# Performance work log

Measured on AMD Instinct MI355X. Metric: run time of the kernel, lower is better.

Reference implementation:

```python
import jax, jax.numpy as jnp
import numpy as np

BN_EPS = 1e-5

def _conv1x1(h, w, b):
    # h: [N, Cin, L], w: [Cout, Cin], b: [Cout] -> [N, Cout, L]
    return jnp.einsum('ncl,oc->nol', h, w) + b[None, :, None]

def _bn_eval(h, g, bt, m, v):
    return (h - m[None, :, None]) / jnp.sqrt(v[None, :, None] + BN_EPS) * g[None, :, None] + bt[None, :, None]

def setup_inputs() -> dict:
    key = jax.random.key(0)
    ks = jax.random.split(key, 20)
    B, R, L, F = 1024, 16, 12, 16
    num_cat, num_cont, V, D = 8, 8, 1000, 32
    FD = F * D  # 512
    H1, H2 = 64, 32
    s = 0.05
    idx_part = jax.random.randint(ks[0], (B, R, L, num_cat), 0, V).astype(jnp.float32)
    cont_part = jax.random.normal(ks[1], (B, R, L, num_cont), dtype=jnp.float32)
    x = jnp.concatenate([idx_part, cont_part], axis=-1)
    return {
        'x': x,
        'cat_emb': jax.random.normal(ks[2], (num_cat, V, D), dtype=jnp.float32) * s,
        'cat_lin': jax.random.normal(ks[3], (num_cat, V, D), dtype=jnp.float32) * s,
        'cont_w': jax.random.normal(ks[4], (num_cont, D), dtype=jnp.float32) * s,
        'cont_b': jax.random.normal(ks[5], (num_cont, D), dtype=jnp.float32) * s,
        'cont_lin_w': jax.random.normal(ks[6], (num_cont, D), dtype=jnp.float32) * s,
        'cont_lin_b': jax.random.normal(ks[7], (num_cont, D), dtype=jnp.float32) * s,
        'fin_bias': jnp.zeros((D,), dtype=jnp.float32),
        'dnn1_w': jax.random.normal(ks[8], (H1, FD), dtype=jnp.float32) * s,
        'dnn1_b': jnp.zeros((H1,), dtype=jnp.float32),
        'bn1_g': jnp.ones((H1,), dtype=jnp.float32),
        'bn1_bt': jnp.zeros((H1,), dtype=jnp.float32),
        'bn1_m': jnp.zeros((H1,), dtype=jnp.float32),
        'bn1_v': jnp.ones((H1,), dtype=jnp.float32),
        'dnn2_w': jax.random.normal(ks[9], (H2, H1), dtype=jnp.float32) * s,
        'dnn2_b': jnp.zeros((H2,), dtype=jnp.float32),
        'bn2_g': jnp.ones((H2,), dtype=jnp.float32),
        'bn2_bt': jnp.zeros((H2,), dtype=jnp.float32),
        'bn2_m': jnp.zeros((H2,), dtype=jnp.float32),
        'bn2_v': jnp.ones((H2,), dtype=jnp.float32),
        'out_w': jax.random.normal(ks[10], (D, H2), dtype=jnp.float32) * s,
        'out_b': jnp.zeros((D,), dtype=jnp.float32),
    }

def reference(x, cat_emb, cat_lin, cont_w, cont_b, cont_lin_w, cont_lin_b, fin_bias,
              dnn1_w, dnn1_b, bn1_g, bn1_bt, bn1_m, bn1_v,
              dnn2_w, dnn2_b, bn2_g, bn2_bt, bn2_m, bn2_v,
              out_w, out_b):
    B, R, L, F = x.shape
    N = B * R
    num_cat = cat_emb.shape[0]
    D = cat_emb.shape[2]
    xf = x.reshape(N, L, F)
    idx = xf[:, :, :num_cat].astype(jnp.int32)   # [N, L, C]
    cont = xf[:, :, num_cat:]                    # [N, L, J]
    f_ids = jnp.arange(num_cat)[None, None, :]   # broadcast field ids
    # embedding path -> [N, D, field, L]
    cat_e = cat_emb[f_ids, idx].transpose(0, 3, 2, 1)                                   # [N,D,C,L]
    cont_e = (cont[..., None] * cont_w[None, None] + cont_b[None, None]).transpose(0, 3, 2, 1)  # [N,D,J,L]
    emb_all = jnp.concatenate([cat_e, cont_e], axis=2)                                  # [N,D,F,L]
    # FM second-order interaction
    ssum = emb_all.sum(axis=2)
    fm = 0.5 * (ssum * ssum - (emb_all * emb_all).sum(axis=2))                          # [N,D,L]
    # linear terms
    cat_l = cat_lin[f_ids, idx].transpose(0, 3, 2, 1)
    cont_l = (cont[..., None] * cont_lin_w[None, None] + cont_lin_b[None, None]).transpose(0, 3, 2, 1)
    linear_terms = cat_l.sum(axis=2) + cont_l.sum(axis=2) + fin_bias[None, :, None]     # [N,D,L]
    # DNN over field-major concatenated channels [N, F*D, L]
    dnn_in = emb_all.transpose(0, 2, 1, 3).reshape(N, F * D, L)
    h = jax.nn.relu(_bn_eval(_conv1x1(dnn_in, dnn1_w, dnn1_b), bn1_g, bn1_bt, bn1_m, bn1_v))
    h = jax.nn.relu(_bn_eval(_conv1x1(h, dnn2_w, dnn2_b), bn2_g, bn2_bt, bn2_m, bn2_v))
    dnn_out = _conv1x1(h, out_w, out_b)                                                 # [N,D,L]
    out = linear_terms + fm + dnn_out
    return out.transpose(0, 2, 1)  # [N, L, D]
```

## Files before the change

kernel.cpp:

```cpp
#include <hip/hip_runtime.h>
#include <hip/hip_bf16.h>

typedef __attribute__((ext_vector_type(8))) short short8;
typedef __attribute__((ext_vector_type(4))) float f32x4;
typedef __attribute__((ext_vector_type(4))) unsigned short ushort4n;

#define BLK 256
#define NTILES 6144

#define A1_OFF   0
#define A2_OFF   0
#define A3_OFF   4096
#define FMC_OFF  18432
#define XS_OFF   18432
#define PART_OFF 26880
#define SMEM_BYTES 35072

#define WS_B1F  0
#define WS_B2F  256
#define WS_W1F  512
#define WS_W2F  37888
#define WS_W3F  41984
#define WS_WFM  44032
#define WS_EL   49152

__global__ void prep_kernel(
    const float* __restrict__ w1, const float* __restrict__ b1,
    const float* __restrict__ g1, const float* __restrict__ bt1,
    const float* __restrict__ m1, const float* __restrict__ v1,
    const float* __restrict__ w2, const float* __restrict__ b2,
    const float* __restrict__ g2, const float* __restrict__ bt2,
    const float* __restrict__ m2, const float* __restrict__ v2,
    const float* __restrict__ w3,
    const float* __restrict__ cat_emb, const float* __restrict__ cat_lin,
    const float* __restrict__ cont_w,  const float* __restrict__ cont_b,
    const float* __restrict__ cont_lw, const float* __restrict__ cont_lb,
    const float* __restrict__ fin_bias,
    float* __restrict__ bias1f, float* __restrict__ bias2f,
    __hip_bfloat16* __restrict__ W1f, __hip_bfloat16* __restrict__ W2f,
    __hip_bfloat16* __restrict__ W3f, __hip_bfloat16* __restrict__ WFMf,
    float2* __restrict__ EL)
{
    int t  = blockIdx.x * blockDim.x + threadIdx.x;
    int nt = gridDim.x * blockDim.x;
    if (t < 64) {
        float s = g1[t] / sqrtf(v1[t] + 1e-5f);
        float cbsum = 0.f;
        for (int f = 0; f < 8; ++f)
            for (int d = 0; d < 32; ++d)
                cbsum += w1[t * 512 + 256 + f * 32 + d] * cont_b[f * 32 + d];
        bias1f[t] = (b1[t] + cbsum - m1[t]) * s + bt1[t];
    }
    if (t >= 64 && t < 96) {
        int o = t - 64;
        float s = g2[o] / sqrtf(v2[o] + 1e-5f);
        bias2f[o] = (b2[o] - m2[o]) * s + bt2[o];
    }
    for (int i = t; i < 8 * 1000 * 32; i += nt) {
        float2 v; v.x = cat_emb[i]; v.y = cat_lin[i];
        EL[i] = v;
    }
    for (int fi = t; fi < 4 * 9 * 512; fi += nt) {
        int j = fi & 7, lane = (fi >> 3) & 63, t2 = fi >> 9;
        int kk = t2 % 9, ct = t2 / 9;
        int k = kk * 32 + ((lane >> 4) << 3) + j;
        int n = ct * 16 + (lane & 15);
        float s = g1[n] / sqrtf(v1[n] + 1e-5f);
        float val = 0.f;
        if (k < 256) val = s * w1[n * 512 + k];
        else if (k < 264) {
            int f = k - 256; float a = 0.f;
            for (int d = 0; d < 32; ++d)
                a += w1[n * 512 + 256 + f * 32 + d] * cont_w[f * 32 + d];
            val = s * a;
        }
        W1f[fi] = __float2bfloat16(val);
    }
    for (int fi = t; fi < 2048; fi += nt) {
        int j = fi & 7, lane = (fi >> 3) & 63, fmct = fi >> 9;
        int kl = ((lane >> 4) << 3) + j;
        int col = fmct * 16 + (lane & 15);
        int d = col & 31, s = col >> 5;
        float val = 0.f;
        if (s == 0) {
            if (kl < 8) val = cont_w[kl * 32 + d];
            else if (kl == 16) { float a = 0.f; for (int f = 0; f < 8; ++f) a += cont_b[f * 32 + d]; val = a; }
        } else {
            if (kl < 8) val = cont_lw[kl * 32 + d] - cont_w[kl * 32 + d] * cont_b[kl * 32 + d];
            else if (kl < 16) { float w = cont_w[(kl - 8) * 32 + d]; val = -0.5f * w * w; }
            else if (kl == 16) {
                float a = fin_bias[d];
                for (int f = 0; f < 8; ++f)
                    a += cont_lb[f * 32 + d] - 0.5f * cont_b[f * 32 + d] * cont_b[f * 32 + d];
                val = a;
            }
        }
        WFMf[fi] = __float2bfloat16(val);
    }
    for (int fi = t; fi < 2048; fi += nt) {
        int j = fi & 7, lane = (fi >> 3) & 63, kt = fi >> 9;
        int ct = kt >> 1, kk = kt & 1;
        int k = kk * 32 + ((lane >> 4) << 3) + j;
        int n = ct * 16 + (lane & 15);
        float s = g2[n] / sqrtf(v2[n] + 1e-5f);
        W2f[fi] = __float2bfloat16(s * w2[n * 64 + k]);
    }
    for (int fi = t; fi < 1024; fi += nt) {
        int j = fi & 7, lane = (fi >> 3) & 63, ct = fi >> 9;
        int k = ((lane >> 4) << 3) + j;
        int n = ct * 16 + (lane & 15);
        W3f[fi] = __float2bfloat16(w3[n * 32 + k]);
    }
}

static __device__ __forceinline__ unsigned short bf16bits(float f) {
    __hip_bfloat16 h = __float2bfloat16(f);
    return *(unsigned short*)&h;
}

__global__ __launch_bounds__(BLK, 4) void fused_kernel(
    const float* __restrict__ x,
    const float* __restrict__ bias1f, const float* __restrict__ bias2f,
    const float* __restrict__ out_b,
    const __hip_bfloat16* __restrict__ W1f,
    const __hip_bfloat16* __restrict__ W2f,
    const __hip_bfloat16* __restrict__ W3f,
    const __hip_bfloat16* __restrict__ WFMf,
    const float2* __restrict__ EL,
    float* __restrict__ out)
{
    __shared__ __align__(16) char smem[SMEM_BYTES];
    const int tid  = threadIdx.x;
    const int lane = tid & 63;
    const int wv   = tid >> 6;
    const int tile = blockIdx.x;
    const int rt2 = wv >> 1, ct2 = wv & 1;

    if (tid < 128)
        ((float4*)(smem + XS_OFF))[tid] = ((const float4*)(x + (size_t)tile * 512))[tid];
    __syncthreads();

    {
        const int p = tid >> 3, d0 = (tid & 7) << 2, g = d0 >> 3, rtp = p >> 4;
        const float* xs = (const float*)(smem + XS_OFF) + p * 16;
        float4 xi0 = ((const float4*)xs)[0];
        float4 xi1 = ((const float4*)xs)[1];
        float4 xc0 = ((const float4*)xs)[2];
        float4 xc1 = ((const float4*)xs)[3];
        float idxf[8] = {xi0.x, xi0.y, xi0.z, xi0.w, xi1.x, xi1.y, xi1.z, xi1.w};
        float cf[8]   = {xc0.x, xc0.y, xc0.z, xc0.w, xc1.x, xc1.y, xc1.z, xc1.w};

        float4 ssum = {0.f, 0.f, 0.f, 0.f};
        float4 lin  = {0.f, 0.f, 0.f, 0.f};
        float4 ssq  = {0.f, 0.f, 0.f, 0.f};

        char* aw = smem + A1_OFF + rtp * 1024 + ((p & 15) + 16 * g) * 16 + (d0 & 7) * 2;
        #pragma unroll
        for (int f = 0; f < 8; ++f) {
            int ix = (int)idxf[f];
            const float4* src = (const float4*)(EL + ((f * 1000 + ix) * 32 + d0));
            float4 v0 = src[0], v1 = src[1];
            float4 e  = {v0.x, v0.z, v1.x, v1.z};
            float4 el = {v0.y, v0.w, v1.y, v1.w};
            ssum += e; ssq += e * e; lin += el;
            ushort4n ev = {bf16bits(e.x), bf16bits(e.y), bf16bits(e.z), bf16bits(e.w)};
            *(ushort4n*)(aw + f * 2048) = ev;
        }
        {
            char* c8 = smem + A1_OFF + 8 * 2048 + rtp * 1024 + ((p & 15) + 16 * g) * 16;
            ushort4n lo = {0, 0, 0, 0}, hi = {0, 0, 0, 0};
            if (g == 0) {
                lo = (ushort4n){bf16bits(cf[0]), bf16bits(cf[1]), bf16bits(cf[2]), bf16bits(cf[3])};
                hi = (ushort4n){bf16bits(cf[4]), bf16bits(cf[5]), bf16bits(cf[6]), bf16bits(cf[7])};
            } else if (g == 1) {
                lo = (ushort4n){bf16bits(cf[0]*cf[0]), bf16bits(cf[1]*cf[1]), bf16bits(cf[2]*cf[2]), bf16bits(cf[3]*cf[3])};
                hi = (ushort4n){bf16bits(cf[4]*cf[4]), bf16bits(cf[5]*cf[5]), bf16bits(cf[6]*cf[6]), bf16bits(cf[7]*cf[7])};
            } else if (g == 2) {
                lo = (ushort4n){0x3F80, 0, 0, 0};
            }
            *(ushort4n*)c8 = lo;
            *(ushort4n*)(c8 + 8) = hi;
        }
        float4 G;
        G.x = lin.x - 0.5f * ssq.x; G.y = lin.y - 0.5f * ssq.y;
        G.z = lin.z - 0.5f * ssq.z; G.w = lin.w - 0.5f * ssq.w;
        float4 o0 = {ssum.x, G.x, ssum.y, G.y};
        float4 o1 = {ssum.z, G.z, ssum.w, G.w};
        *(float4*)(smem + PART_OFF + (p * 32 + d0) * 8)      = o0;
        *(float4*)(smem + PART_OFF + (p * 32 + d0) * 8 + 16) = o1;
    }
    __syncthreads();

    const short8* W1v  = (const short8*)W1f;
    const short8* WFMv = (const short8*)WFMf;
    f32x4 ah0 = {0,0,0,0}, ah1 = {0,0,0,0};
    f32x4 fm0 = {0,0,0,0}, fm1 = {0,0,0,0};
    #pragma unroll
    for (int kk = 0; kk < 9; ++kk) {
        short8 b  = W1v[(wv * 9 + kk) * 64 + lane];
        short8 a0 = *(const short8*)(smem + A1_OFF + kk * 2048 + lane * 16);
        short8 a1 = *(const short8*)(smem + A1_OFF + kk * 2048 + 1024 + lane * 16);
        ah0 = __builtin_amdgcn_mfma_f32_16x16x32_bf16(a0, b, ah0, 0, 0, 0);
        ah1 = __builtin_amdgcn_mfma_f32_16x16x32_bf16(a1, b, ah1, 0, 0, 0);
        if (kk == 8) {
            short8 bfm = WFMv[wv * 64 + lane];
            fm0 = __builtin_amdgcn_mfma_f32_16x16x32_bf16(a0, bfm, fm0, 0, 0, 0);
            fm1 = __builtin_amdgcn_mfma_f32_16x16x32_bf16(a1, bfm, fm1, 0, 0, 0);
        }
    }
    __syncthreads();

    {
        const float bo1 = bias1f[wv * 16 + (lane & 15)];
        const int coll = (wv * 16 + (lane & 15)) & 31;
        const int kk2 = wv >> 1;
        const int nsub = coll >> 3;
        const int jof = (coll & 7) * 2;
        const int rbase = (lane >> 4) << 2;
        #pragma unroll
        for (int rt = 0; rt < 2; ++rt) {
            f32x4 acc = rt ? ah1 : ah0;
            #pragma unroll
            for (int r = 0; r < 4; ++r) {
                float h = fmaxf(acc[r] + bo1, 0.f);
                *(__hip_bfloat16*)(smem + A2_OFF + (kk2 * 2 + rt) * 1024 + ((rbase + r) + 16 * nsub) * 16 + jof)
                    = __float2bfloat16(h);
            }
        }
        const int colf = wv * 16 + (lane & 15);
        const int d = colf & 31, s = colf >> 5;
        #pragma unroll
        for (int rt = 0; rt < 2; ++rt) {
            f32x4 acc = rt ? fm1 : fm0;
            #pragma unroll
            for (int r = 0; r < 4; ++r) {
                int row = rt * 16 + rbase + r;
                *(float*)(smem + FMC_OFF + (row * 66 + d * 2 + s) * 4) = acc[r];
            }
        }
    }
    __syncthreads();

    const short8* W2v = (const short8*)W2f;
    f32x4 acc2 = {0,0,0,0};
    {
        short8 b0 = W2v[(ct2 * 2 + 0) * 64 + lane];
        short8 b1 = W2v[(ct2 * 2 + 1) * 64 + lane];
        short8 a0 = *(const short8*)(smem + A2_OFF + (0 * 2 + rt2) * 1024 + lane * 16);
        acc2 = __builtin_amdgcn_mfma_f32_16x16x32_bf16(a0, b0, acc2, 0, 0, 0);
        short8 a1 = *(const short8*)(smem + A2_OFF + (1 * 2 + rt2) * 1024 + lane * 16);
        acc2 = __builtin_amdgcn_mfma_f32_16x16x32_bf16(a1, b1, acc2, 0, 0, 0);
    }
    {
        const float bo2 = bias2f[ct2 * 16 + (lane & 15)];
        const int col2 = ct2 * 16 + (lane & 15);
        const int nsub2 = col2 >> 3;
        const int jof = (col2 & 7) * 2;
        const int rbase = (lane >> 4) << 2;
        #pragma unroll
        for (int r = 0; r < 4; ++r) {
            float h = fmaxf(acc2[r] + bo2, 0.f);
            *(__hip_bfloat16*)(smem + A3_OFF + rt2 * 1024 + ((rbase + r) + 16 * nsub2) * 16 + jof)
                = __float2bfloat16(h);
        }
    }
    __syncthreads();

    {
        const short8* W3v = (const short8*)W3f;
        short8 b3 = W3v[ct2 * 64 + lane];
        short8 a3 = *(const short8*)(smem + A3_OFF + rt2 * 1024 + lane * 16);
        f32x4 z = {0,0,0,0};
        f32x4 acc3 = __builtin_amdgcn_mfma_f32_16x16x32_bf16(a3, b3, z, 0, 0, 0);

        const int dcol = ct2 * 16 + (lane & 15);
        const float ob = out_b[dcol];
        const int rbase = (lane >> 4) << 2;
        size_t outbase = (size_t)tile * 1024;
        #pragma unroll
        for (int r = 0; r < 4; ++r) {
            int p = rt2 * 16 + rbase + r;
            float2 sg = *(const float2*)(smem + FMC_OFF + (p * 66 + dcol * 2) * 4);
            float2 pc = *(const float2*)(smem + PART_OFF + (p * 32 + dcol) * 8);
            float S = pc.x + sg.x;
            out[outbase + p * 32 + dcol] = acc3[r] + ob + pc.y + sg.y + 0.5f * S * S;
        }
    }
}

extern "C" void kernel_launch(void* const* d_in, const int* in_sizes, int n_in,
                              void* d_out, int out_size, void* d_ws, size_t ws_size,
                              hipStream_t stream) {
    const float* x        = (const float*)d_in[0];
    const float* cat_emb  = (const float*)d_in[1];
    const float* cat_lin  = (const float*)d_in[2];
    const float* cont_w   = (const float*)d_in[3];
    const float* cont_b   = (const float*)d_in[4];
    const float* cont_lw  = (const float*)d_in[5];
    const float* cont_lb  = (const float*)d_in[6];
    const float* fin_bias = (const float*)d_in[7];
    const float* dnn1_w   = (const float*)d_in[8];
    const float* dnn1_b   = (const float*)d_in[9];
    const float* bn1_g    = (const float*)d_in[10];
    const float* bn1_bt   = (const float*)d_in[11];
    const float* bn1_m    = (const float*)d_in[12];
    const float* bn1_v    = (const float*)d_in[13];
    const float* dnn2_w   = (const float*)d_in[14];
    const float* dnn2_b   = (const float*)d_in[15];
    const float* bn2_g    = (const float*)d_in[16];
    const float* bn2_bt   = (const float*)d_in[17];
    const float* bn2_m    = (const float*)d_in[18];
    const float* bn2_v    = (const float*)d_in[19];
    const float* out_w    = (const float*)d_in[20];
    const float* out_b    = (const float*)d_in[21];

    char* ws = (char*)d_ws;
    float* bias1f = (float*)(ws + WS_B1F);
    float* bias2f = (float*)(ws + WS_B2F);
    __hip_bfloat16* W1f  = (__hip_bfloat16*)(ws + WS_W1F);
    __hip_bfloat16* W2f  = (__hip_bfloat16*)(ws + WS_W2F);
    __hip_bfloat16* W3f  = (__hip_bfloat16*)(ws + WS_W3F);
    __hip_bfloat16* WFMf = (__hip_bfloat16*)(ws + WS_WFM);
    float2* EL = (float2*)(ws + WS_EL);

    hipLaunchKernelGGL(prep_kernel, dim3(256), dim3(BLK), 0, stream,
                       dnn1_w, dnn1_b, bn1_g, bn1_bt, bn1_m, bn1_v,
                       dnn2_w, dnn2_b, bn2_g, bn2_bt, bn2_m, bn2_v,
                       out_w, cat_emb, cat_lin, cont_w, cont_b, cont_lw, cont_lb,
                       fin_bias, bias1f, bias2f, W1f, W2f, W3f, WFMf, EL);

    hipLaunchKernelGGL(fused_kernel, dim3(NTILES), dim3(BLK), 0, stream,
                       x, bias1f, bias2f, out_b, W1f, W2f, W3f, WFMf, EL,
                       (float*)d_out);
}
```

Before: 47.24 us.

## Pack embedding tables as interleaved bf16 pairs and shrink shared memory for occupancy

The interleaved embedding/linear table is now stored as packed bf16 pairs in one 32-bit word instead of float2. This halves gather traffic per field and lets the bf16 embedding bits go straight into the MMA operand buffer without a conversion. Shared memory regions are reordered to overlap more tightly, cutting the per-block footprint, and launch bounds are raised to 5 blocks per CU. The trade-off is lower precision for the FM sums and linear terms, which are now computed from bf16-rounded values, plus tighter register limits.

```diff
diff --git a/kernel.cpp b/kernel.cpp
--- a/kernel.cpp
+++ b/kernel.cpp
@@ -9,12 +9,12 @@
 #define NTILES 6144
 
 #define A1_OFF   0
-#define A2_OFF   0
-#define A3_OFF   4096
-#define FMC_OFF  18432
-#define XS_OFF   18432
-#define PART_OFF 26880
-#define SMEM_BYTES 35072
+#define FMC_OFF  0
+#define A2_OFF   8448
+#define A3_OFF   12544
+#define PART_OFF 18432
+#define XS_OFF   26624
+#define SMEM_BYTES 28672
 
 #define WS_B1F  0
 #define WS_B2F  256
@@ -39,7 +39,7 @@
     float* __restrict__ bias1f, float* __restrict__ bias2f,
     __hip_bfloat16* __restrict__ W1f, __hip_bfloat16* __restrict__ W2f,
     __hip_bfloat16* __restrict__ W3f, __hip_bfloat16* __restrict__ WFMf,
-    float2* __restrict__ EL)
+    unsigned* __restrict__ ELb)
 {
     int t  = blockIdx.x * blockDim.x + threadIdx.x;
     int nt = gridDim.x * blockDim.x;
@@ -57,8 +57,11 @@
         bias2f[o] = (b2[o] - m2[o]) * s + bt2[o];
     }
     for (int i = t; i < 8 * 1000 * 32; i += nt) {
-        float2 v; v.x = cat_emb[i]; v.y = cat_lin[i];
-        EL[i] = v;
+        __hip_bfloat16 eb = __float2bfloat16(cat_emb[i]);
+        __hip_bfloat16 lb = __float2bfloat16(cat_lin[i]);
+        unsigned eu = *(unsigned short*)&eb;
+        unsigned lu = *(unsigned short*)&lb;
+        ELb[i] = eu | (lu << 16);
     }
     for (int fi = t; fi < 4 * 9 * 512; fi += nt) {
         int j = fi & 7, lane = (fi >> 3) & 63, t2 = fi >> 9;
@@ -118,7 +121,7 @@
     return *(unsigned short*)&h;
 }
 
-__global__ __launch_bounds__(BLK, 4) void fused_kernel(
+__global__ __launch_bounds__(BLK, 5) void fused_kernel(
     const float* __restrict__ x,
     const float* __restrict__ bias1f, const float* __restrict__ bias2f,
     const float* __restrict__ out_b,
@@ -126,7 +129,7 @@
     const __hip_bfloat16* __restrict__ W2f,
     const __hip_bfloat16* __restrict__ W3f,
     const __hip_bfloat16* __restrict__ WFMf,
-    const float2* __restrict__ EL,
+    const unsigned* __restrict__ ELb,
     float* __restrict__ out)
 {
     __shared__ __align__(16) char smem[SMEM_BYTES];
@@ -158,12 +161,17 @@
         #pragma unroll
         for (int f = 0; f < 8; ++f) {
             int ix = (int)idxf[f];
-            const float4* src = (const float4*)(EL + ((f * 1000 + ix) * 32 + d0));
-            float4 v0 = src[0], v1 = src[1];
-            float4 e  = {v0.x, v0.z, v1.x, v1.z};
-            float4 el = {v0.y, v0.w, v1.y, v1.w};
-            ssum += e; ssq += e * e; lin += el;
-            ushort4n ev = {bf16bits(e.x), bf16bits(e.y), bf16bits(e.z), bf16bits(e.w)};
+            uint4 v = *(const uint4*)(ELb + ((f * 1000 + ix) * 32 + d0));
+            float e0 = __uint_as_float(v.x << 16), l0 = __uint_as_float(v.x & 0xFFFF0000u);
+            float e1 = __uint_as_float(v.y << 16), l1 = __uint_as_float(v.y & 0xFFFF0000u);
+            float e2 = __uint_as_float(v.z << 16), l2 = __uint_as_float(v.z & 0xFFFF0000u);
+            float e3 = __uint_as_float(v.w << 16), l3 = __uint_as_float(v.w & 0xFFFF0000u);
+            ssum.x += e0; ssum.y += e1; ssum.z += e2; ssum.w += e3;
+            ssq.x = fmaf(e0, e0, ssq.x); ssq.y = fmaf(e1, e1, ssq.y);
+            ssq.z = fmaf(e2, e2, ssq.z); ssq.w = fmaf(e3, e3, ssq.w);
+            lin.x += l0; lin.y += l1; lin.z += l2; lin.w += l3;
+            ushort4n ev = {(unsigned short)v.x, (unsigned short)v.y,
+                           (unsigned short)v.z, (unsigned short)v.w};
             *(ushort4n*)(aw + f * 2048) = ev;
         }
         {
@@ -321,15 +329,15 @@
     __hip_bfloat16* W2f  = (__hip_bfloat16*)(ws + WS_W2F);
     __hip_bfloat16* W3f  = (__hip_bfloat16*)(ws + WS_W3F);
     __hip_bfloat16* WFMf = (__hip_bfloat16*)(ws + WS_WFM);
-    float2* EL = (float2*)(ws + WS_EL);
+    unsigned* ELb = (unsigned*)(ws + WS_EL);
 
     hipLaunchKernelGGL(prep_kernel, dim3(256), dim3(BLK), 0, stream,
                        dnn1_w, dnn1_b, bn1_g, bn1_bt, bn1_m, bn1_v,
                        dnn2_w, dnn2_b, bn2_g, bn2_bt, bn2_m, bn2_v,
                        out_w, cat_emb, cat_lin, cont_w, cont_b, cont_lw, cont_lb,
-                       fin_bias, bias1f, bias2f, W1f, W2f, W3f, WFMf, EL);
+                       fin_bias, bias1f, bias2f, W1f, W2f, W3f, WFMf, ELb);
 
     hipLaunchKernelGGL(fused_kernel, dim3(NTILES), dim3(BLK), 0, stream,
-                       x, bias1f, bias2f, out_b, W1f, W2f, W3f, WFMf, EL,
+                       x, bias1f, bias2f, out_b, W1f, W2f, W3f, WFMf, ELb,
                        (float*)d_out);
 }
```

Result: faster. 40.97 us (-13.3%).
